# Performance work log

Hardware: AMD Instinct MI355X
Metric: run time of the kernel (lower is better)

## Reference

```python
import jax, jax.numpy as jnp
import numpy as np

N_NODES = 100_000
N_EDGES = 1_000_000
N_GRAPHS = 2048
F_IN, N_HEADS, HEAD_DIM = 128, 2, 32
NEG_SLOPE = 0.2


def seg_softmax(logits, seg, num):
    # numerically stable scatter-softmax over segments (leading axis)
    m = jax.ops.segment_max(logits, seg, num_segments=num)
    e = jnp.exp(logits - m[seg])
    s = jax.ops.segment_sum(e, seg, num_segments=num)
    return e / s[seg]


def setup_inputs() -> dict:
    key = jax.random.key(0)
    ks = jax.random.split(key, 10)
    HC = N_HEADS * HEAD_DIM
    x = jax.random.normal(ks[0], (N_NODES, F_IN), jnp.float32)
    edge_index = jax.random.randint(ks[1], (2, N_EDGES), 0, N_NODES, jnp.int32)
    batch = jnp.sort(jax.random.randint(ks[2], (N_NODES,), 0, N_GRAPHS, jnp.int32))
    sc_in = 1.0 / np.sqrt(F_IN)
    sc_hc = 1.0 / np.sqrt(HC)
    W_l = jax.random.normal(ks[3], (F_IN, HC), jnp.float32) * sc_in
    W_r = jax.random.normal(ks[4], (F_IN, HC), jnp.float32) * sc_in
    att = jax.random.normal(ks[5], (N_HEADS, HEAD_DIM), jnp.float32) * (1.0 / np.sqrt(HEAD_DIM))
    bias = jnp.zeros((HC,), jnp.float32)
    w_rel = jax.random.normal(ks[6], (HC,), jnp.float32) * sc_hc
    w_root = jax.random.normal(ks[7], (HC,), jnp.float32) * sc_hc
    b_score = jnp.zeros((1,), jnp.float32)
    return {"x": x, "edge_index": edge_index, "batch": batch, "W_l": W_l,
            "W_r": W_r, "att": att, "bias": bias, "w_rel": w_rel,
            "w_root": w_root, "b_score": b_score}


def reference(x, edge_index, batch, W_l, W_r, att, bias, w_rel, w_root, b_score):
    N = x.shape[0]
    H, C = att.shape
    src, dst = edge_index[0], edge_index[1]
    # --- GATv2Conv (add_self_loops=True, concat heads, negative_slope=0.2) ---
    loop = jnp.arange(N, dtype=src.dtype)
    s = jnp.concatenate([src, loop])  # source j
    d = jnp.concatenate([dst, loop])  # target i
    xl = (x @ W_l).reshape(N, H, C)   # lin_l -> source features
    xr = (x @ W_r).reshape(N, H, C)   # lin_r -> target features
    e = jax.nn.leaky_relu(xl[s] + xr[d], NEG_SLOPE)       # [E', H, C]
    logits = jnp.einsum('ehc,hc->eh', e, att)              # [E', H]
    alpha = seg_softmax(logits, d, N)                      # softmax over incoming edges per target
    h = jax.ops.segment_sum(xl[s] * alpha[:, :, None], d, num_segments=N)
    h = h.reshape(N, H * C) + bias                         # conv output (data.x)
    # --- SAGPooling(min_score=-1): softmax(GraphConv score) keeps all nodes ---
    aggr = jax.ops.segment_sum(h[src], dst, num_segments=N)  # GraphConv neighbor add-aggr
    score = aggr @ w_rel + h @ w_root + b_score              # [N]
    sm = seg_softmax(score, batch, N_GRAPHS)
    px = h * sm[:, None]
    # --- global_add_pool + global_mean_pool ---
    add = jax.ops.segment_sum(px, batch, num_segments=N_GRAPHS)
    cnt = jax.ops.segment_sum(jnp.ones((N,), px.dtype), batch, num_segments=N_GRAPHS)
    mean = add / jnp.maximum(cnt, 1.0)[:, None]
    return add + mean  # global_emb [N_GRAPHS, H*C]
```

## Files before the change

### kernel.cpp

```cpp
#include <hip/hip_runtime.h>
#include <hip/hip_bf16.h>

#define N_NODES 100000
#define N_EDGES 1000000
#define N_GRAPHS 2048
#define F_IN 128
#define NEG_SLOPE 0.2f
#define E_TOT (N_EDGES + N_NODES)
#define SCAN_BLK 98
#define GEMM_BLOCKS 782
#define HIST_BLOCKS ((E_TOT + 255) / 256)
#define NODE_BLOCKS ((N_NODES + 255) / 256)

typedef short  bf16x8 __attribute__((ext_vector_type(8)));
typedef float  f32x16 __attribute__((ext_vector_type(16)));

__device__ __forceinline__ short f2bf(float f) {
    unsigned u = __float_as_uint(f);
    unsigned r = (u + 0x7fffu + ((u >> 16) & 1u)) >> 16;
    return (short)r;
}
__device__ __forceinline__ float bf2f(short h) {
    return __uint_as_float(((unsigned)(unsigned short)h) << 16);
}

template <int CTRL>
__device__ __forceinline__ float dpp_add(float x) {
    return x + __int_as_float(__builtin_amdgcn_update_dpp(
        0, __float_as_int(x), CTRL, 0xf, 0xf, true));
}
__device__ __forceinline__ float head_sum_bcast(float x) {
    x = dpp_add<0x111>(x);
    x = dpp_add<0x112>(x);
    x = dpp_add<0x114>(x);
    x = dpp_add<0x118>(x);
    x = dpp_add<0x142>(x);
    return __int_as_float(__builtin_amdgcn_ds_swizzle(__float_as_int(x), 0x03E0));
}
__device__ __forceinline__ float full_sum64(float x) {
    x = dpp_add<0x111>(x);
    x = dpp_add<0x112>(x);
    x = dpp_add<0x114>(x);
    x = dpp_add<0x118>(x);
    x = dpp_add<0x142>(x);
    x = dpp_add<0x143>(x);
    return x;
}
__device__ __forceinline__ float quad_sum(float x) {
    x = dpp_add<0xB1>(x);
    x = dpp_add<0x4E>(x);
    return x;
}

__global__ __launch_bounds__(256) void k_gemm_hist(const float* __restrict__ x,
                                                   const float* __restrict__ Wl,
                                                   const float* __restrict__ Wr,
                                                   const int* __restrict__ ei,
                                                   float* __restrict__ xlr,
                                                   int* __restrict__ counts,
                                                   int* __restrict__ rank_) {
    if (blockIdx.x >= GEMM_BLOCKS) {
        int e = (blockIdx.x - GEMM_BLOCKS) * 256 + threadIdx.x;
        if (e < E_TOT) {
            int d = (e < N_EDGES) ? ei[N_EDGES + e] : (e - N_EDGES);
            rank_[e] = atomicAdd(&counts[d], 1);
        }
        return;
    }
    __shared__ short wt[2][128][136];
    int tid = threadIdx.x;
    {
        int k  = tid >> 1;
        int cq = tid & 1;
        const float* Wsrc = cq ? Wr : Wl;
#pragma unroll
        for (int u = 0; u < 16; ++u) {
            int c0 = u * 4;
            float4 wv = *(const float4*)(Wsrc + (size_t)k * 64 + c0);
            float vv[4] = {wv.x, wv.y, wv.z, wv.w};
#pragma unroll
            for (int q = 0; q < 4; ++q) {
                int c = cq * 64 + c0 + q;
                short hi = f2bf(vv[q]);
                wt[0][c][k] = hi;
                wt[1][c][k] = f2bf(vv[q] - bf2f(hi));
            }
        }
    }
    __syncthreads();
    int lane = tid & 63, w = tid >> 6;
    int m = lane & 31, half = lane >> 5;
    int row = blockIdx.x * 128 + w * 32 + m;
    bool rv = row < N_NODES;
    const float* xrow = x + (size_t)(rv ? row : 0) * F_IN;
    f32x16 acc[4];
#pragma unroll
    for (int t = 0; t < 4; ++t)
#pragma unroll
        for (int i = 0; i < 16; ++i) acc[t][i] = 0.f;

#pragma unroll
    for (int kt = 0; kt < 8; ++kt) {
        int kb = kt * 16 + half * 8;
        float4 xa = rv ? *(const float4*)(xrow + kb)
                       : make_float4(0.f, 0.f, 0.f, 0.f);
        float4 xb = rv ? *(const float4*)(xrow + kb + 4)
                       : make_float4(0.f, 0.f, 0.f, 0.f);
        float xs[8] = {xa.x, xa.y, xa.z, xa.w, xb.x, xb.y, xb.z, xb.w};
        bf16x8 ahi, alo;
#pragma unroll
        for (int j = 0; j < 8; ++j) {
            short hi = f2bf(xs[j]);
            ahi[j] = hi;
            alo[j] = f2bf(xs[j] - bf2f(hi));
        }
#pragma unroll
        for (int t = 0; t < 4; ++t) {
            int n = t * 32 + m;
            bf16x8 bhi = *(const bf16x8*)&wt[0][n][kb];
            bf16x8 blo = *(const bf16x8*)&wt[1][n][kb];
            acc[t] = __builtin_amdgcn_mfma_f32_32x32x16_bf16(ahi, bhi, acc[t], 0, 0, 0);
            acc[t] = __builtin_amdgcn_mfma_f32_32x32x16_bf16(ahi, blo, acc[t], 0, 0, 0);
            acc[t] = __builtin_amdgcn_mfma_f32_32x32x16_bf16(alo, bhi, acc[t], 0, 0, 0);
        }
    }
    int r0 = blockIdx.x * 128 + w * 32 + 4 * half;
#pragma unroll
    for (int t = 0; t < 4; ++t)
#pragma unroll
        for (int reg = 0; reg < 16; ++reg) {
            int rr = r0 + (reg & 3) + 8 * (reg >> 2);
            if (rr < N_NODES)
                xlr[(size_t)rr * 128 + t * 32 + m] = acc[t][reg];
        }
}

__global__ __launch_bounds__(256) void k_scanA(const int* __restrict__ counts,
                                               int* __restrict__ rowptr,
                                               int* __restrict__ bsum) {
    __shared__ int sh[256];
    int t = threadIdx.x, b = blockIdx.x;
    int base = b * 1024 + t * 4;
    int v[4]; int s = 0;
#pragma unroll
    for (int i = 0; i < 4; ++i) {
        int idx = base + i;
        v[i] = (idx < N_NODES) ? counts[idx] : 0;
        s += v[i];
    }
    sh[t] = s; __syncthreads();
    for (int off = 1; off < 256; off <<= 1) {
        int xv = (t >= off) ? sh[t - off] : 0;
        __syncthreads();
        sh[t] += xv;
        __syncthreads();
    }
    int run = sh[t] - s;
    if (t == 255) bsum[b] = sh[255];
#pragma unroll
    for (int i = 0; i < 4; ++i) {
        int idx = base + i;
        if (idx < N_NODES) rowptr[idx] = run;
        run += v[i];
    }
}

__global__ __launch_bounds__(256) void k_scanC_bounds(int* __restrict__ rowptr,
                                                      const int* __restrict__ bsum,
                                                      const int* __restrict__ batch,
                                                      int* __restrict__ start) {
    if (blockIdx.x < NODE_BLOCKS) {
        int i = blockIdx.x * 256 + threadIdx.x;
        int target = blockIdx.x >> 2;
        int lane = threadIdx.x & 63;
        int p = 0;
        if (lane < target)                    p  = bsum[lane];
        if (lane + 64 < target && lane + 64 < SCAN_BLK) p += bsum[lane + 64];
#pragma unroll
        for (int o = 1; o < 64; o <<= 1) p += __shfl_xor(p, o, 64);
        if (i < N_NODES) rowptr[i] += p;
        if (blockIdx.x == 0 && threadIdx.x == 0) rowptr[N_NODES] = E_TOT;
    } else {
        int i = (blockIdx.x - NODE_BLOCKS) * 256 + threadIdx.x;
        if (i >= N_NODES) return;
        int bi = batch[i];
        int bp = (i == 0) ? -1 : batch[i - 1];
        for (int g = bp + 1; g <= bi; ++g) start[g] = i;
        if (i == N_NODES - 1)
            for (int g = bi + 1; g <= N_GRAPHS; ++g) start[g] = N_NODES;
    }
}

__global__ __launch_bounds__(256) void k_scatter(const int* __restrict__ ei,
                                                 const int* __restrict__ rowptr,
                                                 const int* __restrict__ rank_,
                                                 int* __restrict__ sorted_src) {
    int e = blockIdx.x * 256 + threadIdx.x;
    if (e >= E_TOT) return;
    int s, d;
    if (e < N_EDGES) { s = ei[e]; d = ei[N_EDGES + e]; }
    else             { s = d = e - N_EDGES; }
    sorted_src[rowptr[d] + rank_[e]] = s;
}

__global__ __launch_bounds__(256) void k_gat(const float* __restrict__ xlr,
                                             const int* __restrict__ rowptr,
                                             const int* __restrict__ sorted_src,
                                             const float* __restrict__ att,
                                             const float* __restrict__ bias,
                                             const float* __restrict__ w_rel,
                                             const float* __restrict__ w_root,
                                             float* __restrict__ hfeat,
                                             float* __restrict__ tbuf,
                                             float* __restrict__ rbuf) {
    int lane = threadIdx.x & 63;
    int du = __builtin_amdgcn_readfirstlane(blockIdx.x * 4 + (threadIdx.x >> 6));
    if (du >= N_NODES) return;
    float xr_l  = xlr[(size_t)du * 128 + 64 + lane];
    float att_l = att[lane];
    int j0 = __builtin_amdgcn_readfirstlane(rowptr[du]);
    int j1 = __builtin_amdgcn_readfirstlane(rowptr[du + 1]);
    float wsum = 0.f, acc = 0.f;
    int jc = j0;
    for (; jc + 8 <= j1; jc += 8) {
        int sv = sorted_src[jc + (lane & 7)];
        float p[8], xv[8];
#pragma unroll
        for (int i = 0; i < 8; ++i) {
            int s = __builtin_amdgcn_readlane(sv, i);
            xv[i] = (xlr + (size_t)(unsigned)s * 128)[lane];
        }
#pragma unroll
        for (int i = 0; i < 8; ++i) {
            float v = xv[i] + xr_l;
            v = (v > 0.f) ? v : NEG_SLOPE * v;
            p[i] = v * att_l;
        }
#pragma unroll
        for (int i = 0; i < 8; ++i)
            p[i] = head_sum_bcast(p[i]);
#pragma unroll
        for (int i = 0; i < 8; ++i) {
            float w = __expf(p[i]);
            wsum += w;
            acc += w * xv[i];
        }
    }
    for (; jc < j1; jc += 4) {
        int n = j1 - jc;
        int jj = jc + (lane & 3);
        if (jj > j1 - 1) jj = j1 - 1;
        int sv = sorted_src[jj];
        float p[4], xv[4];
#pragma unroll
        for (int i = 0; i < 4; ++i) {
            int s = __builtin_amdgcn_readlane(sv, i);
            xv[i] = (xlr + (size_t)(unsigned)s * 128)[lane];
        }
#pragma unroll
        for (int i = 0; i < 4; ++i) {
            float v = xv[i] + xr_l;
            v = (v > 0.f) ? v : NEG_SLOPE * v;
            p[i] = v * att_l;
        }
#pragma unroll
        for (int i = 0; i < 4; ++i)
            p[i] = head_sum_bcast(p[i]);
#pragma unroll
        for (int i = 0; i < 4; ++i) {
            float w = (i < n) ? __expf(p[i]) : 0.f;
            wsum += w;
            acc += w * xv[i];
        }
    }
    float h = acc / wsum + bias[lane];
    hfeat[(size_t)du * 64 + lane] = h;
    float a = full_sum64(h * w_rel[lane]);
    float b = full_sum64(h * w_root[lane]);
    if (lane == 63) { tbuf[du] = a; rbuf[du] = b; }
}

__global__ __launch_bounds__(256) void k_pool(const int* __restrict__ rowptr,
                                              const int* __restrict__ sorted_src,
                                              const float* __restrict__ t,
                                              const float* __restrict__ r,
                                              const float* __restrict__ b_score,
                                              float* __restrict__ score,
                                              const float* __restrict__ h,
                                              const int* __restrict__ start,
                                              float* __restrict__ out) {
    __shared__ float sh[4];
    __shared__ float shacc[4][64];
    int g = blockIdx.x;
    int tid = threadIdx.x, w = tid >> 6, lane = tid & 63;
    int n0 = start[g], n1 = start[g + 1];
    int cnt = n1 - n0;
    if (cnt <= 0) { if (tid < 64) out[(size_t)g * 64 + tid] = 0.f; return; }
    float bsc = b_score[0];
    for (int base = n0; base < n1; base += 64) {
        int i = base + (tid >> 2);
        float sum = 0.f;
        int jj0 = 0, jj1 = 0;
        if (i < n1) { jj0 = rowptr[i]; jj1 = rowptr[i + 1]; }
        for (int j = jj0 + (tid & 3); j < jj1; j += 4)
            sum += t[sorted_src[j]];
        sum = quad_sum(sum);
        if (i < n1 && (tid & 3) == 0)
            score[i] = sum - t[i] + r[i] + bsc;
    }
    __syncthreads();
    float m = -1e30f;
    for (int i = n0 + tid; i < n1; i += 256) m = fmaxf(m, score[i]);
#pragma unroll
    for (int o = 32; o; o >>= 1) m = fmaxf(m, __shfl_xor(m, o, 64));
    if (lane == 0) sh[w] = m;
    __syncthreads();
    m = fmaxf(fmaxf(sh[0], sh[1]), fmaxf(sh[2], sh[3]));
    float ssum = 0.f;
    for (int i = n0 + tid; i < n1; i += 256) ssum += __expf(score[i] - m);
#pragma unroll
    for (int o = 32; o; o >>= 1) ssum += __shfl_xor(ssum, o, 64);
    __syncthreads();
    if (lane == 0) sh[w] = ssum;
    __syncthreads();
    ssum = sh[0] + sh[1] + sh[2] + sh[3];
    float acc = 0.f;
    for (int i = n0 + w; i < n1; i += 4)
        acc += __expf(score[i] - m) * h[(size_t)i * 64 + lane];
    shacc[w][lane] = acc;
    __syncthreads();
    if (w == 0) {
        float tot = shacc[0][lane] + shacc[1][lane] + shacc[2][lane] + shacc[3][lane];
        out[(size_t)g * 64 + lane] = tot * (1.f + 1.f / (float)cnt) / ssum;
    }
}

extern "C" void kernel_launch(void* const* d_in, const int* in_sizes, int n_in,
                              void* d_out, int out_size, void* d_ws, size_t ws_size,
                              hipStream_t stream) {
    const float* x      = (const float*)d_in[0];
    const int*   ei     = (const int*)d_in[1];
    const int*   batch  = (const int*)d_in[2];
    const float* Wl     = (const float*)d_in[3];
    const float* Wr     = (const float*)d_in[4];
    const float* att    = (const float*)d_in[5];
    const float* bias   = (const float*)d_in[6];
    const float* w_rel  = (const float*)d_in[7];
    const float* w_root = (const float*)d_in[8];
    const float* b_sc   = (const float*)d_in[9];

    char* ws = (char*)d_ws;
    size_t off = 0;
    auto alloc = [&](size_t bytes) { void* p = ws + off; off += (bytes + 255) & ~255ull; return p; };
    float* xlr        = (float*)alloc((size_t)N_NODES * 128 * 4);
    float* hfeat      = (float*)alloc((size_t)N_NODES * 64 * 4);
    int*   sorted_src = (int*)  alloc((size_t)E_TOT * 4);
    int*   rank_      = (int*)  alloc((size_t)E_TOT * 4);
    int*   counts     = (int*)  alloc((size_t)N_NODES * 4);
    int*   rowptr     = (int*)  alloc((size_t)(N_NODES + 1) * 4);
    int*   bsum       = (int*)  alloc((size_t)SCAN_BLK * 4);
    float* tbuf       = (float*)alloc((size_t)N_NODES * 4);
    float* rbuf       = (float*)alloc((size_t)N_NODES * 4);
    float* score      = (float*)alloc((size_t)N_NODES * 4);
    int*   start      = (int*)  alloc((size_t)(N_GRAPHS + 1) * 4);

    (void)hipMemsetAsync(counts, 0, (size_t)N_NODES * 4, stream);

    k_gemm_hist   <<<GEMM_BLOCKS + HIST_BLOCKS, 256, 0, stream>>>(x, Wl, Wr, ei, xlr, counts, rank_);
    k_scanA       <<<SCAN_BLK, 256, 0, stream>>>(counts, rowptr, bsum);
    k_scanC_bounds<<<NODE_BLOCKS * 2, 256, 0, stream>>>(rowptr, bsum, batch, start);
    k_scatter     <<<(E_TOT + 255) / 256, 256, 0, stream>>>(ei, rowptr, rank_, sorted_src);
    k_gat         <<<(N_NODES + 3) / 4, 256, 0, stream>>>(xlr, rowptr, sorted_src, att, bias,
                                                          w_rel, w_root, hfeat, tbuf, rbuf);
    k_pool        <<<N_GRAPHS, 256, 0, stream>>>(rowptr, sorted_src, tbuf, rbuf, b_sc,
                                                 score, hfeat, start, (float*)d_out);
}
```

Baseline: 253.3 us.

## Replace global-atomic CSR build with two-level bucketed counting sort

Global atomics on per-node counts are replaced by a bucketed counting sort. Edges are first binned into buckets of 64 destination nodes using LDS histograms per block, then a column prefix and a small scan set bucket bases, and edges are scattered into packed bucket arrays. A per-bucket fine pass then produces rowptr and sorted_src. This removes contended global atomics and the per-edge rank array, at the cost of more kernel launches, a serial column-prefix loop over 1075 blocks per bucket, and the GEMM no longer running concurrently with the histogram.

Result: slower. 384.4 us (+51.8%).

```diff
diff --git a/kernel.cpp b/kernel.cpp
--- a/kernel.cpp
+++ b/kernel.cpp
@@ -7,10 +7,11 @@
 #define F_IN 128
 #define NEG_SLOPE 0.2f
 #define E_TOT (N_EDGES + N_NODES)
-#define SCAN_BLK 98
 #define GEMM_BLOCKS 782
-#define HIST_BLOCKS ((E_TOT + 255) / 256)
-#define NODE_BLOCKS ((N_NODES + 255) / 256)
+#define NODE_BLOCKS 391
+#define NB 1563
+#define EB 1075
+#define CP_BLOCKS 7
 
 typedef short  bf16x8 __attribute__((ext_vector_type(8)));
 typedef float  f32x16 __attribute__((ext_vector_type(16)));
@@ -52,21 +53,10 @@
     return x;
 }
 
-__global__ __launch_bounds__(256) void k_gemm_hist(const float* __restrict__ x,
-                                                   const float* __restrict__ Wl,
-                                                   const float* __restrict__ Wr,
-                                                   const int* __restrict__ ei,
-                                                   float* __restrict__ xlr,
-                                                   int* __restrict__ counts,
-                                                   int* __restrict__ rank_) {
-    if (blockIdx.x >= GEMM_BLOCKS) {
-        int e = (blockIdx.x - GEMM_BLOCKS) * 256 + threadIdx.x;
-        if (e < E_TOT) {
-            int d = (e < N_EDGES) ? ei[N_EDGES + e] : (e - N_EDGES);
-            rank_[e] = atomicAdd(&counts[d], 1);
-        }
-        return;
-    }
+__global__ __launch_bounds__(256) void k_gemm(const float* __restrict__ x,
+                                              const float* __restrict__ Wl,
+                                              const float* __restrict__ Wr,
+                                              float* __restrict__ xlr) {
     __shared__ short wt[2][128][136];
     int tid = threadIdx.x;
     {
@@ -135,18 +125,61 @@
         }
 }
 
-__global__ __launch_bounds__(256) void k_scanA(const int* __restrict__ counts,
-                                               int* __restrict__ rowptr,
-                                               int* __restrict__ bsum) {
+__global__ __launch_bounds__(256) void k_bhist(const int* __restrict__ ei,
+                                               int* __restrict__ bhist) {
+    __shared__ int lh[NB];
+    int tid = threadIdx.x, b = blockIdx.x;
+    for (int i = tid; i < NB; i += 256) lh[i] = 0;
+    __syncthreads();
+    int e0 = b * 1024;
+#pragma unroll
+    for (int j = 0; j < 4; ++j) {
+        int e = e0 + j * 256 + tid;
+        if (e < E_TOT) {
+            int d = (e < N_EDGES) ? ei[N_EDGES + e] : (e - N_EDGES);
+            atomicAdd(&lh[d >> 6], 1);
+        }
+    }
+    __syncthreads();
+    for (int i = tid; i < NB; i += 256) bhist[(size_t)b * NB + i] = lh[i];
+}
+
+__global__ __launch_bounds__(256) void k_colprefix_bounds(int* __restrict__ bhist,
+                                                          int* __restrict__ colsum,
+                                                          const int* __restrict__ batch,
+                                                          int* __restrict__ start) {
+    if (blockIdx.x < CP_BLOCKS) {
+        int i = blockIdx.x * 256 + threadIdx.x;
+        if (i >= NB) return;
+        int run = 0;
+#pragma unroll 4
+        for (int b = 0; b < EB; ++b) {
+            int t = bhist[(size_t)b * NB + i];
+            bhist[(size_t)b * NB + i] = run;
+            run += t;
+        }
+        colsum[i] = run;
+    } else {
+        int i = (blockIdx.x - CP_BLOCKS) * 256 + threadIdx.x;
+        if (i >= N_NODES) return;
+        int bi = batch[i];
+        int bp = (i == 0) ? -1 : batch[i - 1];
+        for (int g = bp + 1; g <= bi; ++g) start[g] = i;
+        if (i == N_NODES - 1)
+            for (int g = bi + 1; g <= N_GRAPHS; ++g) start[g] = N_NODES;
+    }
+}
+
+__global__ __launch_bounds__(256) void k_cbscan(const int* __restrict__ colsum,
+                                                int* __restrict__ colbase) {
     __shared__ int sh[256];
-    int t = threadIdx.x, b = blockIdx.x;
-    int base = b * 1024 + t * 4;
-    int v[4]; int s = 0;
-#pragma unroll
-    for (int i = 0; i < 4; ++i) {
-        int idx = base + i;
-        v[i] = (idx < N_NODES) ? counts[idx] : 0;
-        s += v[i];
+    int t = threadIdx.x;
+    int v[7]; int s = 0;
+#pragma unroll
+    for (int k = 0; k < 7; ++k) {
+        int idx = t * 7 + k;
+        v[k] = (idx < NB) ? colsum[idx] : 0;
+        s += v[k];
     }
     sh[t] = s; __syncthreads();
     for (int off = 1; off < 256; off <<= 1) {
@@ -156,51 +189,70 @@
         __syncthreads();
     }
     int run = sh[t] - s;
-    if (t == 255) bsum[b] = sh[255];
-#pragma unroll
-    for (int i = 0; i < 4; ++i) {
-        int idx = base + i;
-        if (idx < N_NODES) rowptr[idx] = run;
-        run += v[i];
-    }
-}
-
-__global__ __launch_bounds__(256) void k_scanC_bounds(int* __restrict__ rowptr,
-                                                      const int* __restrict__ bsum,
-                                                      const int* __restrict__ batch,
-                                                      int* __restrict__ start) {
-    if (blockIdx.x < NODE_BLOCKS) {
-        int i = blockIdx.x * 256 + threadIdx.x;
-        int target = blockIdx.x >> 2;
-        int lane = threadIdx.x & 63;
-        int p = 0;
-        if (lane < target)                    p  = bsum[lane];
-        if (lane + 64 < target && lane + 64 < SCAN_BLK) p += bsum[lane + 64];
-#pragma unroll
-        for (int o = 1; o < 64; o <<= 1) p += __shfl_xor(p, o, 64);
-        if (i < N_NODES) rowptr[i] += p;
-        if (blockIdx.x == 0 && threadIdx.x == 0) rowptr[N_NODES] = E_TOT;
-    } else {
-        int i = (blockIdx.x - NODE_BLOCKS) * 256 + threadIdx.x;
-        if (i >= N_NODES) return;
-        int bi = batch[i];
-        int bp = (i == 0) ? -1 : batch[i - 1];
-        for (int g = bp + 1; g <= bi; ++g) start[g] = i;
-        if (i == N_NODES - 1)
-            for (int g = bi + 1; g <= N_GRAPHS; ++g) start[g] = N_NODES;
-    }
-}
-
-__global__ __launch_bounds__(256) void k_scatter(const int* __restrict__ ei,
-                                                 const int* __restrict__ rowptr,
-                                                 const int* __restrict__ rank_,
-                                                 int* __restrict__ sorted_src) {
-    int e = blockIdx.x * 256 + threadIdx.x;
-    if (e >= E_TOT) return;
-    int s, d;
-    if (e < N_EDGES) { s = ei[e]; d = ei[N_EDGES + e]; }
-    else             { s = d = e - N_EDGES; }
-    sorted_src[rowptr[d] + rank_[e]] = s;
+#pragma unroll
+    for (int k = 0; k < 7; ++k) {
+        int idx = t * 7 + k;
+        if (idx <= NB) colbase[idx] = run;
+        run += v[k];
+    }
+}
+
+__global__ __launch_bounds__(256) void k_bscatter(const int* __restrict__ ei,
+                                                  const int* __restrict__ bhist,
+                                                  const int* __restrict__ colbase,
+                                                  int* __restrict__ bpack) {
+    __shared__ int lh[NB];
+    int tid = threadIdx.x, b = blockIdx.x;
+    for (int i = tid; i < NB; i += 256) lh[i] = 0;
+    __syncthreads();
+    int e0 = b * 1024;
+#pragma unroll
+    for (int j = 0; j < 4; ++j) {
+        int e = e0 + j * 256 + tid;
+        if (e < E_TOT) {
+            int s, d;
+            if (e < N_EDGES) { s = ei[e]; d = ei[N_EDGES + e]; }
+            else             { s = d = e - N_EDGES; }
+            int bk = d >> 6;
+            int lr = atomicAdd(&lh[bk], 1);
+            int pos = colbase[bk] + bhist[(size_t)b * NB + bk] + lr;
+            bpack[pos] = s | ((d & 63) << 17);
+        }
+    }
+}
+
+__global__ __launch_bounds__(256) void k_fine(const int* __restrict__ bpack,
+                                              const int* __restrict__ colbase,
+                                              int* __restrict__ rowptr,
+                                              int* __restrict__ sorted_src) {
+    __shared__ int fcnt[64];
+    __shared__ int foff[64];
+    int i = blockIdx.x, tid = threadIdx.x;
+    int cb0 = colbase[i], cb1 = colbase[i + 1];
+    if (tid < 64) fcnt[tid] = 0;
+    __syncthreads();
+    for (int e = cb0 + tid; e < cb1; e += 256)
+        atomicAdd(&fcnt[bpack[e] >> 17], 1);
+    __syncthreads();
+    if (tid < 64) {
+        int v = fcnt[tid];
+        int inc = v;
+#pragma unroll
+        for (int o = 1; o < 64; o <<= 1) {
+            int t = __shfl_up(inc, o, 64);
+            if (tid >= o) inc += t;
+        }
+        int excl = inc - v;
+        foff[tid] = excl;
+        int node = i * 64 + tid;
+        if (node <= N_NODES) rowptr[node] = cb0 + excl;
+    }
+    __syncthreads();
+    for (int e = cb0 + tid; e < cb1; e += 256) {
+        int w = bpack[e];
+        int lr = atomicAdd(&foff[w >> 17], 1);
+        sorted_src[cb0 + lr] = w & 131071;
+    }
 }
 
 __global__ __launch_bounds__(256) void k_gat(const float* __restrict__ xlr,
@@ -354,24 +406,25 @@
     auto alloc = [&](size_t bytes) { void* p = ws + off; off += (bytes + 255) & ~255ull; return p; };
     float* xlr        = (float*)alloc((size_t)N_NODES * 128 * 4);
     float* hfeat      = (float*)alloc((size_t)N_NODES * 64 * 4);
+    int*   bhist      = (int*)hfeat;
+    int*   bpack      = (int*)  alloc((size_t)E_TOT * 4);
     int*   sorted_src = (int*)  alloc((size_t)E_TOT * 4);
-    int*   rank_      = (int*)  alloc((size_t)E_TOT * 4);
-    int*   counts     = (int*)  alloc((size_t)N_NODES * 4);
     int*   rowptr     = (int*)  alloc((size_t)(N_NODES + 1) * 4);
-    int*   bsum       = (int*)  alloc((size_t)SCAN_BLK * 4);
+    int*   colsum     = (int*)  alloc((size_t)NB * 4);
+    int*   colbase    = (int*)  alloc((size_t)(NB + 1) * 4);
     float* tbuf       = (float*)alloc((size_t)N_NODES * 4);
     float* rbuf       = (float*)alloc((size_t)N_NODES * 4);
     float* score      = (float*)alloc((size_t)N_NODES * 4);
     int*   start      = (int*)  alloc((size_t)(N_GRAPHS + 1) * 4);
 
-    (void)hipMemsetAsync(counts, 0, (size_t)N_NODES * 4, stream);
-
-    k_gemm_hist   <<<GEMM_BLOCKS + HIST_BLOCKS, 256, 0, stream>>>(x, Wl, Wr, ei, xlr, counts, rank_);
-    k_scanA       <<<SCAN_BLK, 256, 0, stream>>>(counts, rowptr, bsum);
-    k_scanC_bounds<<<NODE_BLOCKS * 2, 256, 0, stream>>>(rowptr, bsum, batch, start);
-    k_scatter     <<<(E_TOT + 255) / 256, 256, 0, stream>>>(ei, rowptr, rank_, sorted_src);
-    k_gat         <<<(N_NODES + 3) / 4, 256, 0, stream>>>(xlr, rowptr, sorted_src, att, bias,
-                                                          w_rel, w_root, hfeat, tbuf, rbuf);
-    k_pool        <<<N_GRAPHS, 256, 0, stream>>>(rowptr, sorted_src, tbuf, rbuf, b_sc,
-                                                 score, hfeat, start, (float*)d_out);
-}
+    k_gemm            <<<GEMM_BLOCKS, 256, 0, stream>>>(x, Wl, Wr, xlr);
+    k_bhist           <<<EB, 256, 0, stream>>>(ei, bhist);
+    k_colprefix_bounds<<<CP_BLOCKS + NODE_BLOCKS, 256, 0, stream>>>(bhist, colsum, batch, start);
+    k_cbscan          <<<1, 256, 0, stream>>>(colsum, colbase);
+    k_bscatter        <<<EB, 256, 0, stream>>>(ei, bhist, colbase, bpack);
+    k_fine            <<<NB, 256, 0, stream>>>(bpack, colbase, rowptr, sorted_src);
+    k_gat             <<<(N_NODES + 3) / 4, 256, 0, stream>>>(xlr, rowptr, sorted_src, att, bias,
+                                                              w_rel, w_root, hfeat, tbuf, rbuf);
+    k_pool            <<<N_GRAPHS, 256, 0, stream>>>(rowptr, sorted_src, tbuf, rbuf, b_sc,
+                                                     score, hfeat, start, (float*)d_out);
+}
```
